# Kernel tuning notes

Hardware: AMD Instinct MI355X
Metric: run time of the kernel (lower is better)

## Reference

```python
import jax, jax.numpy as jnp
import numpy as np

N_ATOMS = 8192
N_FINGERPRINT = 10000
DIM = 64
N_LAYERS = 3
N_MOL = 256


def setup_inputs() -> dict:
    key = jax.random.key(0)
    k1, k2, k3, k4, k5 = jax.random.split(key, 5)
    fingerprints = jax.random.randint(k1, (N_ATOMS,), 0, N_FINGERPRINT)
    adjacencies = jax.random.uniform(k2, (N_ATOMS, N_ATOMS), dtype=jnp.float32)
    segment_ids = jnp.sort(jax.random.randint(k3, (N_ATOMS,), 0, N_MOL))
    embed_table = jax.random.normal(k4, (N_FINGERPRINT, DIM), dtype=jnp.float32) * 0.1
    W = jax.random.normal(k5, (N_LAYERS, DIM, DIM), dtype=jnp.float32) * (1.0 / np.sqrt(DIM))
    b = jnp.zeros((N_LAYERS, DIM), dtype=jnp.float32)
    return {"fingerprints": fingerprints, "adjacencies": adjacencies,
            "segment_ids": segment_ids, "embed_table": embed_table, "W": W, "b": b}


def reference(fingerprints, adjacencies, segment_ids, embed_table, W, b):
    # Embed fingerprint indices -> [N_atoms, dim]
    vectors = embed_table[fingerprints]
    # MPNN layers: h = relu(Linear(v)); v = h + A @ h  (residual message passing)
    for layer in range(N_LAYERS):
        h = jax.nn.relu(jnp.einsum('nd,ed->ne', vectors, W[layer]) + b[layer])
        vectors = h + adjacencies @ h
    # Sum pooling per molecule (torch.split + sum == segment_sum over sorted ids)
    molecular_vectors = jax.ops.segment_sum(vectors, segment_ids, num_segments=N_MOL)
    return molecular_vectors
```

## Files before the change

### kernel.cpp

```cpp
#include <hip/hip_runtime.h>

#define N_ATOMS 8192
#define DIM 64
#define N_MOL 256
#define N_LAYERS 3
#define KS 16
#define KCH (N_ATOMS / KS)
#define BM 128
#define BN 64
#define BK 64
#define NSTEP (KCH / BK)

typedef __attribute__((ext_vector_type(8))) short short8v;
typedef __attribute__((ext_vector_type(4))) float f32x4;
typedef unsigned short ushort_t;

__device__ __forceinline__ ushort_t f2bf(float x) {
    unsigned u = __float_as_uint(x);
    u += 0x7fffu + ((u >> 16) & 1u);
    return (ushort_t)(u >> 16);
}

__device__ __forceinline__ void gload16(const void* gsrc, void* ldst) {
    __builtin_amdgcn_global_load_lds(
        (const __attribute__((address_space(1))) void*)gsrc,
        (__attribute__((address_space(3))) void*)ldst, 16, 0, 0);
}

template <int FIRST>
__global__ __launch_bounds__(256) void fused_linear_kernel(
        const int* __restrict__ fp, const float* __restrict__ table,
        const float* __restrict__ hprev, const float* __restrict__ pbuf,
        const float* __restrict__ W, const float* __restrict__ b,
        float* __restrict__ hout, ushort_t* __restrict__ hT) {
    __shared__ float Ws[DIM][DIM + 1];
    __shared__ float vsT[DIM][36];

    const int t = threadIdx.x;
    const int n0 = blockIdx.x * 32;
    for (int i = t; i < DIM * DIM; i += 256) Ws[i >> 6][i & 63] = W[i];
    for (int i = t; i < 32 * DIM; i += 256) {
        const int nl = i >> 6, d = i & 63;
        const size_t n = n0 + nl;
        float val;
        if (FIRST) {
            val = table[(size_t)fp[n] * DIM + d];
        } else {
            val = hprev[n * DIM + d];
#pragma unroll
            for (int sp = 0; sp < KS; ++sp)
                val += pbuf[(size_t)sp * (N_ATOMS * DIM) + n * DIM + d];
        }
        vsT[d][nl] = val;
    }
    __syncthreads();

    const int e = t & 63;
    const int g = t >> 6;
    float acc[8];
    const float be = b[e];
#pragma unroll
    for (int i = 0; i < 8; ++i) acc[i] = be;

    for (int d = 0; d < DIM; ++d) {
        const float w = Ws[e][d];
        const float4* vp = (const float4*)&vsT[d][g * 8];
        float4 x0 = vp[0], x1 = vp[1];
        acc[0] += w * x0.x; acc[1] += w * x0.y; acc[2] += w * x0.z; acc[3] += w * x0.w;
        acc[4] += w * x1.x; acc[5] += w * x1.y; acc[6] += w * x1.z; acc[7] += w * x1.w;
    }

    ushort_t hb[8];
#pragma unroll
    for (int i = 0; i < 8; ++i) {
        float hv = acc[i] > 0.f ? acc[i] : 0.f;
        hout[(size_t)(n0 + g * 8 + i) * DIM + e] = hv;
        hb[i] = f2bf(hv);
    }
    *(short8v*)(hT + (size_t)e * N_ATOMS + n0 + g * 8) = *(short8v*)&hb[0];
}

template <int CVT>
__global__ __launch_bounds__(256) void matmul_mfma_kernel(
        const float* __restrict__ A, const ushort_t* __restrict__ Abf_in,
        ushort_t* __restrict__ Abf_out, const ushort_t* __restrict__ hT,
        float* __restrict__ pbuf) {
    __shared__ ushort_t Asw[2][BM * BK];
    __shared__ ushort_t Bsw[2][BN * BK];

    const int t  = threadIdx.x;
    const int w  = t >> 6;
    const int l  = t & 63;
    const int lm = l & 15;
    const int lq = l >> 4;
    const int r0 = blockIdx.x * BM;
    const size_t kc0 = (size_t)blockIdx.y * KCH;

    auto stage = [&](int bi, size_t kb) {
        if (CVT) {
#pragma unroll
            for (int q = 0; q < 4; ++q) {
                const int i = q * 256 + t;
                const int r = i >> 3, s = i & 7;
                const size_t goff = (size_t)(r0 + r) * N_ATOMS + kb + s * 8;
                const float4* g = (const float4*)(A + goff);
                float4 a0 = g[0], a1 = g[1];
                short8v vv;
                vv[0] = (short)f2bf(a0.x); vv[1] = (short)f2bf(a0.y);
                vv[2] = (short)f2bf(a0.z); vv[3] = (short)f2bf(a0.w);
                vv[4] = (short)f2bf(a1.x); vv[5] = (short)f2bf(a1.y);
                vv[6] = (short)f2bf(a1.z); vv[7] = (short)f2bf(a1.w);
                *(short8v*)&Asw[bi][r * BK + ((s ^ (r & 7)) << 3)] = vv;
                *(short8v*)(Abf_out + goff) = vv;
            }
        } else {
#pragma unroll
            for (int q = 0; q < 4; ++q) {
                const int i = q * 256 + t;
                const int r = i >> 3, s = i & 7;
                gload16(Abf_in + (size_t)(r0 + r) * N_ATOMS + kb + ((s ^ (r & 7)) << 3),
                        &Asw[bi][(q * 256 + w * 64) * 8]);
            }
        }
#pragma unroll
        for (int q = 0; q < 2; ++q) {
            const int i = q * 256 + t;
            const int r = i >> 3, s = i & 7;
            gload16(hT + (size_t)r * N_ATOMS + kb + ((s ^ (r & 7)) << 3),
                    &Bsw[bi][(q * 256 + w * 64) * 8]);
        }
    };

    f32x4 acc[2][4];
#pragma unroll
    for (int m = 0; m < 2; ++m)
#pragma unroll
        for (int n = 0; n < 4; ++n) acc[m][n] = (f32x4){0.f, 0.f, 0.f, 0.f};

    stage(0, kc0);
    __syncthreads();

    for (int ks = 0; ks < NSTEP; ++ks) {
        const int bi = ks & 1;
        if (ks + 1 < NSTEP) stage(bi ^ 1, kc0 + (size_t)(ks + 1) * BK);
#pragma unroll
        for (int kki = 0; kki < 2; ++kki) {
            const int sx = ((lq + kki * 4) ^ (lm & 7)) << 3;
            const int ra = w * 32 + lm;
            short8v a0 = *(const short8v*)&Asw[bi][ra * BK + sx];
            short8v a1 = *(const short8v*)&Asw[bi][(ra + 16) * BK + sx];
            short8v b0 = *(const short8v*)&Bsw[bi][(lm)      * BK + sx];
            short8v b1 = *(const short8v*)&Bsw[bi][(lm + 16) * BK + sx];
            short8v b2 = *(const short8v*)&Bsw[bi][(lm + 32) * BK + sx];
            short8v b3 = *(const short8v*)&Bsw[bi][(lm + 48) * BK + sx];
            acc[0][0] = __builtin_amdgcn_mfma_f32_16x16x32_bf16(a0, b0, acc[0][0], 0, 0, 0);
            acc[0][1] = __builtin_amdgcn_mfma_f32_16x16x32_bf16(a0, b1, acc[0][1], 0, 0, 0);
            acc[0][2] = __builtin_amdgcn_mfma_f32_16x16x32_bf16(a0, b2, acc[0][2], 0, 0, 0);
            acc[0][3] = __builtin_amdgcn_mfma_f32_16x16x32_bf16(a0, b3, acc[0][3], 0, 0, 0);
            acc[1][0] = __builtin_amdgcn_mfma_f32_16x16x32_bf16(a1, b0, acc[1][0], 0, 0, 0);
            acc[1][1] = __builtin_amdgcn_mfma_f32_16x16x32_bf16(a1, b1, acc[1][1], 0, 0, 0);
            acc[1][2] = __builtin_amdgcn_mfma_f32_16x16x32_bf16(a1, b2, acc[1][2], 0, 0, 0);
            acc[1][3] = __builtin_amdgcn_mfma_f32_16x16x32_bf16(a1, b3, acc[1][3], 0, 0, 0);
        }
        __syncthreads();
    }

    float* pb = pbuf + (size_t)blockIdx.y * ((size_t)N_ATOMS * DIM);
    const int rb = r0 + w * 32 + lq * 4;
#pragma unroll
    for (int m = 0; m < 2; ++m)
#pragma unroll
        for (int j = 0; j < 4; ++j) {
            float* vp = pb + (size_t)(rb + m * 16 + j) * DIM + lm;
#pragma unroll
            for (int n = 0; n < 4; ++n) vp[n * 16] = acc[m][n][j];
        }
}

__device__ __forceinline__ int lower_bound_dev(const int* __restrict__ seg, int val) {
    int lo = 0, hi = N_ATOMS;
    while (lo < hi) {
        int mid = (lo + hi) >> 1;
        if (seg[mid] < val) lo = mid + 1; else hi = mid;
    }
    return lo;
}

__global__ __launch_bounds__(256) void fused_segsum_kernel(
        const float* __restrict__ h, const float* __restrict__ pbuf,
        const int* __restrict__ seg, float* __restrict__ out) {
    __shared__ float sm[4][DIM];
    const int m = blockIdx.x;
    const int d = threadIdx.x & 63;
    const int g = threadIdx.x >> 6;
    const int lo = lower_bound_dev(seg, m);
    const int hi = lower_bound_dev(seg, m + 1);
    float acc = 0.f;
    for (int n = lo + g; n < hi; n += 4) {
        float v = h[(size_t)n * DIM + d];
#pragma unroll
        for (int sp = 0; sp < KS; ++sp)
            v += pbuf[(size_t)sp * (N_ATOMS * DIM) + (size_t)n * DIM + d];
        acc += v;
    }
    sm[g][d] = acc;
    __syncthreads();
    if (g == 0) out[(size_t)m * DIM + d] = sm[0][d] + sm[1][d] + sm[2][d] + sm[3][d];
}

extern "C" void kernel_launch(void* const* d_in, const int* in_sizes, int n_in,
                              void* d_out, int out_size, void* d_ws, size_t ws_size,
                              hipStream_t stream) {
    const int*   fp    = (const int*)d_in[0];
    const float* A     = (const float*)d_in[1];
    const int*   seg   = (const int*)d_in[2];
    const float* table = (const float*)d_in[3];
    const float* W     = (const float*)d_in[4];
    const float* b     = (const float*)d_in[5];
    float* out = (float*)d_out;

    float*    h0   = (float*)d_ws;
    float*    h1   = h0 + (size_t)N_ATOMS * DIM;
    float*    pbuf = h1 + (size_t)N_ATOMS * DIM;
    ushort_t* hT   = (ushort_t*)(pbuf + (size_t)KS * N_ATOMS * DIM);
    ushort_t* Abf  = hT + (size_t)DIM * N_ATOMS;

    dim3 mmgrid(N_ATOMS / BM, KS);

    fused_linear_kernel<1><<<N_ATOMS / 32, 256, 0, stream>>>(
        fp, table, nullptr, pbuf, W, b, h0, hT);
    matmul_mfma_kernel<1><<<mmgrid, 256, 0, stream>>>(A, Abf, Abf, hT, pbuf);
    fused_linear_kernel<0><<<N_ATOMS / 32, 256, 0, stream>>>(
        fp, table, h0, pbuf, W + DIM * DIM, b + DIM, h1, hT);
    matmul_mfma_kernel<0><<<mmgrid, 256, 0, stream>>>(A, Abf, Abf, hT, pbuf);
    fused_linear_kernel<0><<<N_ATOMS / 32, 256, 0, stream>>>(
        fp, table, h1, pbuf, W + 2 * DIM * DIM, b + 2 * DIM, h0, hT);
    matmul_mfma_kernel<0><<<mmgrid, 256, 0, stream>>>(A, Abf, Abf, hT, pbuf);
    fused_segsum_kernel<<<N_MOL, 256, 0, stream>>>(h0, pbuf, seg, out);
}
```

Baseline: 221.9 us.

## Fold segment-sum into last layer by precomputing segment-summed adjacency rows

Uses associativity: segment_sum(A@h) equals (S·A)@h, so a new kernel sums the bf16 adjacency rows per molecule into a 256x8192 matrix SA. The final matmul then runs over 256 rows instead of 8192, and the final kernel adds the per-segment sum of h to the reduced partials. The cost is an extra kernel that reads the whole bf16 adjacency once more, serially per molecule, plus extra bf16 rounding of the summed rows, which can affect accuracy.

Measured after the change: 432.5 us. +94.9%, slower.

```diff
diff --git a/kernel.cpp b/kernel.cpp
--- a/kernel.cpp
+++ b/kernel.cpp
@@ -3,7 +3,6 @@
 #define N_ATOMS 8192
 #define DIM 64
 #define N_MOL 256
-#define N_LAYERS 3
 #define KS 16
 #define KCH (N_ATOMS / KS)
 #define BM 128
@@ -20,11 +19,23 @@
     u += 0x7fffu + ((u >> 16) & 1u);
     return (ushort_t)(u >> 16);
 }
+__device__ __forceinline__ float bf2f(unsigned u) {
+    return __uint_as_float(u << 16);
+}
 
 __device__ __forceinline__ void gload16(const void* gsrc, void* ldst) {
     __builtin_amdgcn_global_load_lds(
         (const __attribute__((address_space(1))) void*)gsrc,
         (__attribute__((address_space(3))) void*)ldst, 16, 0, 0);
+}
+
+__device__ __forceinline__ int lower_bound_dev(const int* __restrict__ seg, int val) {
+    int lo = 0, hi = N_ATOMS;
+    while (lo < hi) {
+        int mid = (lo + hi) >> 1;
+        if (seg[mid] < val) lo = mid + 1; else hi = mid;
+    }
+    return lo;
 }
 
 template <int FIRST>
@@ -177,35 +188,39 @@
         }
 }
 
-__device__ __forceinline__ int lower_bound_dev(const int* __restrict__ seg, int val) {
-    int lo = 0, hi = N_ATOMS;
-    while (lo < hi) {
-        int mid = (lo + hi) >> 1;
-        if (seg[mid] < val) lo = mid + 1; else hi = mid;
-    }
-    return lo;
-}
-
-__global__ __launch_bounds__(256) void fused_segsum_kernel(
-        const float* __restrict__ h, const float* __restrict__ pbuf,
+__global__ __launch_bounds__(256) void sa_kernel(
+        const ushort_t* __restrict__ Abf, const int* __restrict__ seg,
+        ushort_t* __restrict__ SAbf) {
+    const int k  = blockIdx.x * 512 + threadIdx.x * 2;
+    const int m0 = blockIdx.y * 16;
+    for (int mm = 0; mm < 16; ++mm) {
+        const int m = m0 + mm;
+        const int lo = lower_bound_dev(seg, m);
+        const int hi = lower_bound_dev(seg, m + 1);
+        float a0 = 0.f, a1 = 0.f;
+        for (int n = lo; n < hi; ++n) {
+            unsigned v = *(const unsigned*)(Abf + (size_t)n * N_ATOMS + k);
+            a0 += bf2f(v & 0xffffu);
+            a1 += bf2f(v >> 16);
+        }
+        SAbf[(size_t)m * N_ATOMS + k]     = f2bf(a0);
+        SAbf[(size_t)m * N_ATOMS + k + 1] = f2bf(a1);
+    }
+}
+
+__global__ __launch_bounds__(64) void telefinal_kernel(
+        const float* __restrict__ h3, const float* __restrict__ pbuf,
         const int* __restrict__ seg, float* __restrict__ out) {
-    __shared__ float sm[4][DIM];
     const int m = blockIdx.x;
-    const int d = threadIdx.x & 63;
-    const int g = threadIdx.x >> 6;
+    const int d = threadIdx.x;
     const int lo = lower_bound_dev(seg, m);
     const int hi = lower_bound_dev(seg, m + 1);
-    float acc = 0.f;
-    for (int n = lo + g; n < hi; n += 4) {
-        float v = h[(size_t)n * DIM + d];
-#pragma unroll
-        for (int sp = 0; sp < KS; ++sp)
-            v += pbuf[(size_t)sp * (N_ATOMS * DIM) + (size_t)n * DIM + d];
-        acc += v;
-    }
-    sm[g][d] = acc;
-    __syncthreads();
-    if (g == 0) out[(size_t)m * DIM + d] = sm[0][d] + sm[1][d] + sm[2][d] + sm[3][d];
+    float s = 0.f;
+    for (int n = lo; n < hi; ++n) s += h3[(size_t)n * DIM + d];
+#pragma unroll
+    for (int sp = 0; sp < KS; ++sp)
+        s += pbuf[(size_t)sp * (N_ATOMS * DIM) + (size_t)m * DIM + d];
+    out[(size_t)m * DIM + d] = s;
 }
 
 extern "C" void kernel_launch(void* const* d_in, const int* in_sizes, int n_in,
@@ -223,18 +238,21 @@
     float*    h1   = h0 + (size_t)N_ATOMS * DIM;
     float*    pbuf = h1 + (size_t)N_ATOMS * DIM;
     ushort_t* hT   = (ushort_t*)(pbuf + (size_t)KS * N_ATOMS * DIM);
-    ushort_t* Abf  = hT + (size_t)DIM * N_ATOMS;
+    ushort_t* SAbf = hT + (size_t)DIM * N_ATOMS;
+    ushort_t* Abf  = SAbf + (size_t)N_MOL * N_ATOMS;
 
     dim3 mmgrid(N_ATOMS / BM, KS);
 
     fused_linear_kernel<1><<<N_ATOMS / 32, 256, 0, stream>>>(
         fp, table, nullptr, pbuf, W, b, h0, hT);
     matmul_mfma_kernel<1><<<mmgrid, 256, 0, stream>>>(A, Abf, Abf, hT, pbuf);
+    sa_kernel<<<dim3(16, 16), 256, 0, stream>>>(Abf, seg, SAbf);
     fused_linear_kernel<0><<<N_ATOMS / 32, 256, 0, stream>>>(
         fp, table, h0, pbuf, W + DIM * DIM, b + DIM, h1, hT);
     matmul_mfma_kernel<0><<<mmgrid, 256, 0, stream>>>(A, Abf, Abf, hT, pbuf);
     fused_linear_kernel<0><<<N_ATOMS / 32, 256, 0, stream>>>(
         fp, table, h1, pbuf, W + 2 * DIM * DIM, b + 2 * DIM, h0, hT);
-    matmul_mfma_kernel<0><<<mmgrid, 256, 0, stream>>>(A, Abf, Abf, hT, pbuf);
-    fused_segsum_kernel<<<N_MOL, 256, 0, stream>>>(h0, pbuf, seg, out);
-}
+    matmul_mfma_kernel<0><<<dim3(N_MOL / BM, KS), 256, 0, stream>>>(
+        A, SAbf, Abf, hT, pbuf);
+    telefinal_kernel<<<N_MOL, DIM, 0, stream>>>(h0, pbuf, seg, out);
+}
```

## Replace split-K partial buffers with atomicAdd accumulation into residual vector

Applied to the files above, without the earlier changes.

The matmul kernel no longer writes 16 split-K partial slabs that later kernels had to sum. Instead each block atomically adds its partial tile into the vector buffer, which already holds h written by the linear kernel, so the residual h + A@h is formed in place. This removes about 32 MB of partial writes and reads per layer, and the reduction loops in the linear and segsum kernels go away. In exchange it adds float atomic contention (16-way per element) and makes the summation order nondeterministic.

New measurement: 231.7 us. 4.4% more time.

```diff
diff --git a/kernel.cpp b/kernel.cpp
--- a/kernel.cpp
+++ b/kernel.cpp
@@ -3,7 +3,6 @@
 #define N_ATOMS 8192
 #define DIM 64
 #define N_MOL 256
-#define N_LAYERS 3
 #define KS 16
 #define KCH (N_ATOMS / KS)
 #define BM 128
@@ -27,12 +26,21 @@
         (__attribute__((address_space(3))) void*)ldst, 16, 0, 0);
 }
 
+__device__ __forceinline__ int lower_bound_dev(const int* __restrict__ seg, int val) {
+    int lo = 0, hi = N_ATOMS;
+    while (lo < hi) {
+        int mid = (lo + hi) >> 1;
+        if (seg[mid] < val) lo = mid + 1; else hi = mid;
+    }
+    return lo;
+}
+
 template <int FIRST>
 __global__ __launch_bounds__(256) void fused_linear_kernel(
         const int* __restrict__ fp, const float* __restrict__ table,
-        const float* __restrict__ hprev, const float* __restrict__ pbuf,
+        const float* __restrict__ vprev,
         const float* __restrict__ W, const float* __restrict__ b,
-        float* __restrict__ hout, ushort_t* __restrict__ hT) {
+        float* __restrict__ vnext, ushort_t* __restrict__ hT) {
     __shared__ float Ws[DIM][DIM + 1];
     __shared__ float vsT[DIM][36];
 
@@ -43,14 +51,8 @@
         const int nl = i >> 6, d = i & 63;
         const size_t n = n0 + nl;
         float val;
-        if (FIRST) {
-            val = table[(size_t)fp[n] * DIM + d];
-        } else {
-            val = hprev[n * DIM + d];
-#pragma unroll
-            for (int sp = 0; sp < KS; ++sp)
-                val += pbuf[(size_t)sp * (N_ATOMS * DIM) + n * DIM + d];
-        }
+        if (FIRST) val = table[(size_t)fp[n] * DIM + d];
+        else       val = vprev[n * DIM + d];
         vsT[d][nl] = val;
     }
     __syncthreads();
@@ -74,7 +76,7 @@
 #pragma unroll
     for (int i = 0; i < 8; ++i) {
         float hv = acc[i] > 0.f ? acc[i] : 0.f;
-        hout[(size_t)(n0 + g * 8 + i) * DIM + e] = hv;
+        vnext[(size_t)(n0 + g * 8 + i) * DIM + e] = hv;
         hb[i] = f2bf(hv);
     }
     *(short8v*)(hT + (size_t)e * N_ATOMS + n0 + g * 8) = *(short8v*)&hb[0];
@@ -84,7 +86,7 @@
 __global__ __launch_bounds__(256) void matmul_mfma_kernel(
         const float* __restrict__ A, const ushort_t* __restrict__ Abf_in,
         ushort_t* __restrict__ Abf_out, const ushort_t* __restrict__ hT,
-        float* __restrict__ pbuf) {
+        float* __restrict__ vnext) {
     __shared__ ushort_t Asw[2][BM * BK];
     __shared__ ushort_t Bsw[2][BN * BK];
 
@@ -165,30 +167,20 @@
         __syncthreads();
     }
 
-    float* pb = pbuf + (size_t)blockIdx.y * ((size_t)N_ATOMS * DIM);
     const int rb = r0 + w * 32 + lq * 4;
 #pragma unroll
     for (int m = 0; m < 2; ++m)
 #pragma unroll
         for (int j = 0; j < 4; ++j) {
-            float* vp = pb + (size_t)(rb + m * 16 + j) * DIM + lm;
-#pragma unroll
-            for (int n = 0; n < 4; ++n) vp[n * 16] = acc[m][n][j];
-        }
-}
-
-__device__ __forceinline__ int lower_bound_dev(const int* __restrict__ seg, int val) {
-    int lo = 0, hi = N_ATOMS;
-    while (lo < hi) {
-        int mid = (lo + hi) >> 1;
-        if (seg[mid] < val) lo = mid + 1; else hi = mid;
-    }
-    return lo;
-}
-
-__global__ __launch_bounds__(256) void fused_segsum_kernel(
-        const float* __restrict__ h, const float* __restrict__ pbuf,
-        const int* __restrict__ seg, float* __restrict__ out) {
+            float* vp = vnext + (size_t)(rb + m * 16 + j) * DIM + lm;
+#pragma unroll
+            for (int n = 0; n < 4; ++n) atomicAdd(vp + n * 16, acc[m][n][j]);
+        }
+}
+
+__global__ __launch_bounds__(256) void segsum_kernel(
+        const float* __restrict__ v, const int* __restrict__ seg,
+        float* __restrict__ out) {
     __shared__ float sm[4][DIM];
     const int m = blockIdx.x;
     const int d = threadIdx.x & 63;
@@ -196,13 +188,7 @@
     const int lo = lower_bound_dev(seg, m);
     const int hi = lower_bound_dev(seg, m + 1);
     float acc = 0.f;
-    for (int n = lo + g; n < hi; n += 4) {
-        float v = h[(size_t)n * DIM + d];
-#pragma unroll
-        for (int sp = 0; sp < KS; ++sp)
-            v += pbuf[(size_t)sp * (N_ATOMS * DIM) + (size_t)n * DIM + d];
-        acc += v;
-    }
+    for (int n = lo + g; n < hi; n += 4) acc += v[(size_t)n * DIM + d];
     sm[g][d] = acc;
     __syncthreads();
     if (g == 0) out[(size_t)m * DIM + d] = sm[0][d] + sm[1][d] + sm[2][d] + sm[3][d];
@@ -219,22 +205,21 @@
     const float* b     = (const float*)d_in[5];
     float* out = (float*)d_out;
 
-    float*    h0   = (float*)d_ws;
-    float*    h1   = h0 + (size_t)N_ATOMS * DIM;
-    float*    pbuf = h1 + (size_t)N_ATOMS * DIM;
-    ushort_t* hT   = (ushort_t*)(pbuf + (size_t)KS * N_ATOMS * DIM);
-    ushort_t* Abf  = hT + (size_t)DIM * N_ATOMS;
+    float*    vA  = (float*)d_ws;
+    float*    vB  = vA + (size_t)N_ATOMS * DIM;
+    ushort_t* hT  = (ushort_t*)(vB + (size_t)N_ATOMS * DIM);
+    ushort_t* Abf = hT + (size_t)DIM * N_ATOMS;
 
     dim3 mmgrid(N_ATOMS / BM, KS);
 
     fused_linear_kernel<1><<<N_ATOMS / 32, 256, 0, stream>>>(
-        fp, table, nullptr, pbuf, W, b, h0, hT);
-    matmul_mfma_kernel<1><<<mmgrid, 256, 0, stream>>>(A, Abf, Abf, hT, pbuf);
+        fp, table, nullptr, W, b, vA, hT);
+    matmul_mfma_kernel<1><<<mmgrid, 256, 0, stream>>>(A, Abf, Abf, hT, vA);
     fused_linear_kernel<0><<<N_ATOMS / 32, 256, 0, stream>>>(
-        fp, table, h0, pbuf, W + DIM * DIM, b + DIM, h1, hT);
-    matmul_mfma_kernel<0><<<mmgrid, 256, 0, stream>>>(A, Abf, Abf, hT, pbuf);
+        fp, table, vA, W + DIM * DIM, b + DIM, vB, hT);
+    matmul_mfma_kernel<0><<<mmgrid, 256, 0, stream>>>(A, Abf, Abf, hT, vB);
     fused_linear_kernel<0><<<N_ATOMS / 32, 256, 0, stream>>>(
-        fp, table, h1, pbuf, W + 2 * DIM * DIM, b + 2 * DIM, h0, hT);
-    matmul_mfma_kernel<0><<<mmgrid, 256, 0, stream>>>(A, Abf, Abf, hT, pbuf);
-    fused_segsum_kernel<<<N_MOL, 256, 0, stream>>>(h0, pbuf, seg, out);
-}
+        fp, table, vB, W + 2 * DIM * DIM, b + 2 * DIM, vA, hT);
+    matmul_mfma_kernel<0><<<mmgrid, 256, 0, stream>>>(A, Abf, Abf, hT, vA);
+    segsum_kernel<<<N_MOL, 256, 0, stream>>>(vA, seg, out);
+}
```
